# Kernel tuning notes

Hardware: AMD Instinct MI355X
Metric: run time of the kernel (lower is better)

Reference implementation:

```python
import jax, jax.numpy as jnp
import numpy as np
from jax import lax

# Mamba-2 block, mode='recurrent' (chunked SSD scan), default vanilla causal dwconv
D_MODEL = 2048
D_STATE = 64
D_CONV = 4
HEADDIM = 64
EXPAND = 2
NGROUPS = 1
CHUNK = 64
D_INNER = EXPAND * D_MODEL          # 4096
NHEADS = D_INNER // HEADDIM          # 64
CONV_DIM = D_INNER + 2 * NGROUPS * D_STATE   # 4224
D_IN_PROJ = 2 * D_INNER + 2 * NGROUPS * D_STATE + NHEADS  # 8384
BATCH, SEQ = 2, 4096
EPS = 1e-5


def setup_inputs() -> dict:
    key = jax.random.key(0)
    ks = jax.random.split(key, 8)
    x = jax.random.normal(ks[0], (BATCH, SEQ, D_MODEL), jnp.float32)
    in_proj_w = jax.random.normal(ks[1], (D_IN_PROJ, D_MODEL), jnp.float32) / np.sqrt(D_MODEL)
    conv_w = jax.random.normal(ks[2], (CONV_DIM, D_CONV), jnp.float32) / np.sqrt(D_CONV)
    conv_b = jnp.zeros((CONV_DIM,), jnp.float32)
    # dt_bias = inverse-softplus of dt sampled log-uniform in [1e-3, 1e-1]
    dt = jnp.exp(jax.random.uniform(ks[3], (NHEADS,)) * (np.log(0.1) - np.log(0.001)) + np.log(0.001))
    dt_bias = dt + jnp.log(-jnp.expm1(-dt))
    A_log = jnp.log(jax.random.uniform(ks[4], (NHEADS,), minval=1.0, maxval=16.0))
    D = jnp.ones((NHEADS,), jnp.float32)
    norm_w = jnp.ones((D_INNER,), jnp.float32)
    out_proj_w = jax.random.normal(ks[5], (D_MODEL, D_INNER), jnp.float32) / np.sqrt(D_INNER)
    return dict(x=x, in_proj_w=in_proj_w, conv_w=conv_w, conv_b=conv_b,
                dt_bias=dt_bias, A_log=A_log, D=D, norm_w=norm_w, out_proj_w=out_proj_w)


def _segsum(a):
    """a: (..., T) -> (..., T, T) lower-triangular segment sums."""
    T = a.shape[-1]
    cs = jnp.cumsum(a, axis=-1)
    d = cs[..., :, None] - cs[..., None, :]
    mask = jnp.tril(jnp.ones((T, T), dtype=bool))
    return jnp.where(mask, d, -jnp.inf)


def _forward(x, in_proj_w, conv_w, conv_b, dt_bias, A_log, D, norm_w, out_proj_w):
    Bsz, L, _ = x.shape
    nc = L // CHUNK
    zxbcdt = x @ in_proj_w.T                      # (B,L,D_IN_PROJ)
    z = zxbcdt[..., :D_INNER]
    xBC = zxbcdt[..., D_INNER:D_INNER + CONV_DIM]
    dt = zxbcdt[..., D_INNER + CONV_DIM:]         # (B,L,H)

    # causal depthwise conv1d (padding = d_conv-1, sliced to L) + SiLU
    xBC_t = jnp.transpose(xBC, (0, 2, 1))         # (B,C,L)
    y = lax.conv_general_dilated(xBC_t, conv_w[:, None, :], window_strides=(1,),
                                 padding=[(D_CONV - 1, 0)],
                                 feature_group_count=CONV_DIM,
                                 dimension_numbers=('NCH', 'OIH', 'NCH'))
    y = y + conv_b[None, :, None]
    xBC = jax.nn.silu(jnp.transpose(y, (0, 2, 1)))  # (B,L,C)

    xs = xBC[..., :D_INNER]
    Bm = xBC[..., D_INNER:D_INNER + NGROUPS * D_STATE]
    Cm = xBC[..., D_INNER + NGROUPS * D_STATE:]

    dt = jax.nn.softplus(dt + dt_bias)            # (B,L,H)
    A = -jnp.exp(A_log)                           # (H,)
    dA = dt * A                                   # (B,L,H)

    xh = xs.reshape(Bsz, L, NHEADS, HEADDIM)
    Bh = jnp.repeat(Bm.reshape(Bsz, L, NGROUPS, D_STATE), NHEADS // NGROUPS, axis=2)  # (B,L,H,N)
    Ch = jnp.repeat(Cm.reshape(Bsz, L, NGROUPS, D_STATE), NHEADS // NGROUPS, axis=2)
    xdt = xh * dt[..., None]                      # (B,L,H,P)

    # chunk
    Ac = dA.reshape(Bsz, nc, CHUNK, NHEADS).transpose(0, 1, 3, 2)  # (B,c,H,l)
    A_cumsum = jnp.cumsum(Ac, axis=-1)                             # (B,c,H,l)
    Lmat = jnp.exp(_segsum(Ac))                                    # (B,c,H,l,s)
    Cc = Ch.reshape(Bsz, nc, CHUNK, NHEADS, D_STATE)
    Bc = Bh.reshape(Bsz, nc, CHUNK, NHEADS, D_STATE)
    xc = xdt.reshape(Bsz, nc, CHUNK, NHEADS, HEADDIM)

    # intra-chunk (diagonal blocks)
    Y_diag = jnp.einsum('bclhn,bcshn,bchls,bcshp->bclhp', Cc, Bc, Lmat, xc)

    # per-chunk end states
    decay_states = jnp.exp(A_cumsum[..., -1:] - A_cumsum)          # (B,c,H,l)
    states = jnp.einsum('bcshn,bchs,bcshp->bchpn', Bc, decay_states, xc)  # (B,c,H,P,N)
    chunk_decay = jnp.exp(A_cumsum[..., -1])                       # (B,c,H)

    # inter-chunk recurrence over chunks
    def scan_fn(h, inp):
        dec, st = inp                              # (B,H), (B,H,P,N)
        prev = h
        h = dec[..., None, None] * h + st
        return h, prev

    h0 = jnp.zeros((Bsz, NHEADS, HEADDIM, D_STATE), x.dtype)
    _, prev_states = lax.scan(scan_fn, h0,
                              (chunk_decay.transpose(1, 0, 2), states.transpose(1, 0, 2, 3, 4)))
    prev_states = prev_states.transpose(1, 0, 2, 3, 4)             # (B,c,H,P,N)

    Y_off = jnp.einsum('bclhn,bchpn,bchl->bclhp', Cc, prev_states, jnp.exp(A_cumsum))

    Y = (Y_diag + Y_off).reshape(Bsz, L, NHEADS, HEADDIM) + D[:, None] * xh
    yf = Y.reshape(Bsz, L, D_INNER)

    # gated RMSNorm, then out projection
    yf = yf * jax.nn.silu(z)
    yf = yf * lax.rsqrt(jnp.mean(yf * yf, axis=-1, keepdims=True) + EPS) * norm_w
    return yf @ out_proj_w.T


def reference(x, in_proj_w, conv_w, conv_b, dt_bias, A_log, D, norm_w, out_proj_w):
    return _forward(x, in_proj_w, conv_w, conv_b, dt_bias, A_log, D, norm_w, out_proj_w)
```

## Files before the change

kernel.cpp:

```cpp
#include <hip/hip_runtime.h>

#define BATCH 2
#define SEQ 4096
#define DMODEL 2048
#define DINNER 4096
#define NHEADS 64
#define HEADDIM 64
#define DSTATE 64
#define CONVDIM 4224
#define DINPROJ 8384
#define NCHUNK 64
#define CHUNKL 64
#define MROWS (BATCH*SEQ)

typedef __bf16 bf16_t;
typedef bf16_t bf16x8 __attribute__((ext_vector_type(8)));
typedef float f32x4 __attribute__((ext_vector_type(4)));
typedef unsigned short u16;
typedef u16 u16x8 __attribute__((ext_vector_type(8)));

__device__ __forceinline__ u16 f2bf(float f) {
  unsigned int u = __float_as_uint(f);
  u += 0x7fff + ((u >> 16) & 1);
  return (u16)(u >> 16);
}
__device__ __forceinline__ float bf2f(u16 s) {
  return __uint_as_float(((unsigned int)s) << 16);
}

__device__ __forceinline__ void async_load16(const void* g, void* l) {
  __builtin_amdgcn_global_load_lds(
      (const __attribute__((address_space(1))) void*)g,
      (__attribute__((address_space(3))) void*)l, 16, 0, 0);
}

__global__ __launch_bounds__(256) void cvt_kernel(const float* __restrict__ in,
                                                  u16* __restrict__ out, int n4) {
  int i = blockIdx.x * 256 + threadIdx.x;
  if (i >= n4) return;
  float4 v = *(const float4*)(in + (size_t)i * 4);
  ushort4 o;
  o.x = f2bf(v.x); o.y = f2bf(v.y); o.z = f2bf(v.z); o.w = f2bf(v.w);
  *(ushort4*)(out + (size_t)i * 4) = o;
}

template <int EPI>
__global__ __launch_bounds__(512, 2) void gemm_bt(const u16* __restrict__ A,
                                                  const u16* __restrict__ B,
                                                  int M, int N, int K,
                                                  float* __restrict__ outf,
                                                  u16* __restrict__ z_out,
                                                  u16* __restrict__ xe_out,
                                                  float* __restrict__ bce_out,
                                                  float* __restrict__ dt_out) {
  __shared__ char smem[147456];
  const int tid = threadIdx.x;
  const int w = tid >> 6, lane = tid & 63;
  const int id = blockIdx.y * gridDim.x + blockIdx.x;
  const int xcd = id & 7;
  const int q = id >> 3;
  const int m0 = (xcd * 8 + (q & 7)) * 128;
  const int n0 = (q >> 3) * 256;
  const int wr = (w >> 2) * 64, wc = (w & 3) * 64;
  const int fr = lane & 15, fq = lane >> 4;
  const int nkt = K >> 6;

  const u16* aptr[2];
  const u16* bptr[4];
#pragma unroll
  for (int p = 0; p < 2; ++p) {
    int d = p * 8192 + tid * 16;
    int row = d >> 7;
    int colb = (d & 127) ^ ((row & 7) << 4);
    aptr[p] = A + (size_t)(m0 + row) * K + (colb >> 1);
  }
#pragma unroll
  for (int p = 0; p < 4; ++p) {
    int d = p * 8192 + tid * 16;
    int row = d >> 7;
    int colb = (d & 127) ^ ((row & 7) << 4);
    int gn = n0 + row;
    if (gn > N - 1) gn = N - 1;
    bptr[p] = B + (size_t)gn * K + (colb >> 1);
  }

  auto stage_to = [&](int bi) {
    char* base = (char*)smem + bi * 49152;
#pragma unroll
    for (int p = 0; p < 2; ++p) {
      async_load16(aptr[p], base + p * 8192 + tid * 16);
      aptr[p] += 64;
    }
#pragma unroll
    for (int p = 0; p < 4; ++p) {
      async_load16(bptr[p], base + 16384 + p * 8192 + tid * 16);
      bptr[p] += 64;
    }
  };

  auto load_frags = [&](int bi, int ks, bf16x8* af, bf16x8* bf) {
    const char* base = (const char*)smem + bi * 49152;
#pragma unroll
    for (int i = 0; i < 4; ++i) {
      int rowa = wr + i * 16 + fr;
      af[i] = *(const bf16x8*)(base + ((rowa * 128 + ks * 64 + fq * 16) ^ ((fr & 7) << 4)));
      int rowb = wc + i * 16 + fr;
      bf[i] = *(const bf16x8*)(base + 16384 +
                               ((rowb * 128 + ks * 64 + fq * 16) ^ ((fr & 7) << 4)));
    }
  };

  f32x4 acc[4][4];
#pragma unroll
  for (int i = 0; i < 4; ++i)
#pragma unroll
    for (int j = 0; j < 4; ++j) acc[i][j] = (f32x4){0.f, 0.f, 0.f, 0.f};

  stage_to(0);
  stage_to(1);
  asm volatile("s_waitcnt vmcnt(6)" ::: "memory");
  __builtin_amdgcn_s_barrier();

  bf16x8 a0[4], b0[4], a1[4], b1[4];
  load_frags(0, 0, a0, b0);

  int cur = 0;
  for (int t = 0; t < nkt; ++t) {
    int nx = cur + 1; if (nx == 3) nx = 0;
    int st = nx + 1; if (st == 3) st = 0;
    load_frags(cur, 1, a1, b1);
    const bool do_stage = (t + 2 < nkt);
    if (do_stage) stage_to(st);
    __builtin_amdgcn_s_setprio(1);
#pragma unroll
    for (int i = 0; i < 4; ++i)
#pragma unroll
      for (int j = 0; j < 4; ++j)
        acc[i][j] = __builtin_amdgcn_mfma_f32_16x16x32_bf16(a0[i], b0[j], acc[i][j], 0, 0, 0);
    __builtin_amdgcn_s_setprio(0);
    if (do_stage) {
      asm volatile("s_waitcnt vmcnt(6)" ::: "memory");
    } else {
      asm volatile("s_waitcnt vmcnt(0)" ::: "memory");
    }
    __builtin_amdgcn_s_barrier();
    if (t + 1 < nkt) load_frags(nx, 0, a0, b0);
    __builtin_amdgcn_s_setprio(1);
#pragma unroll
    for (int i = 0; i < 4; ++i)
#pragma unroll
      for (int j = 0; j < 4; ++j)
        acc[i][j] = __builtin_amdgcn_mfma_f32_16x16x32_bf16(a1[i], b1[j], acc[i][j], 0, 0, 0);
    __builtin_amdgcn_s_setprio(0);
    cur = nx;
  }

#pragma unroll
  for (int i = 0; i < 4; ++i) {
#pragma unroll
    for (int j = 0; j < 4; ++j) {
#pragma unroll
      for (int rr2 = 0; rr2 < 4; ++rr2) {
        int row = m0 + wr + i * 16 + fq * 4 + rr2;
        int col = n0 + wc + j * 16 + fr;
        float v = acc[i][j][rr2];
        if (EPI == 0) {
          if (col < N) outf[(size_t)row * N + col] = v;
        } else {
          if (col < DINNER) {
            z_out[(size_t)row * DINNER + col] = f2bf(v);
          } else if (col < 2 * DINNER) {
            xe_out[(size_t)row * DINNER + (col - DINNER)] = f2bf(v);
          } else if (col < DINNER + CONVDIM) {
            bce_out[(size_t)row * 128 + (col - 2 * DINNER)] = v;
          } else if (col < DINPROJ) {
            dt_out[(size_t)row * NHEADS + (col - DINNER - CONVDIM)] = v;
          }
        }
      }
    }
  }
}

__global__ __launch_bounds__(64) void dt_acs_kernel(float* __restrict__ dt,
                                                    const float* __restrict__ dt_bias,
                                                    const float* __restrict__ A_log,
                                                    float* __restrict__ Acs) {
  const int bid = blockIdx.x;
  const int h = threadIdx.x;
  const float bias = dt_bias[h];
  const float nA = -expf(A_log[h]);
  float run = 0.f;
  float* acs_row = Acs + ((size_t)bid * 64 + h) * 64;
  for (int s = 0; s < 64; ++s) {
    size_t g = ((size_t)bid * 64 + s) * 64 + h;
    float xv = dt[g] + bias;
    float sp = (xv > 20.f) ? xv : log1pf(expf(xv));
    dt[g] = sp;
    run += nA * sp;
    acs_row[s] = run;
  }
}

__global__ __launch_bounds__(256) void conv_silu_kernel(const u16* __restrict__ xe,
                                                        const float* __restrict__ bce,
                                                        const float* __restrict__ conv_w,
                                                        const float* __restrict__ conv_b,
                                                        u16* __restrict__ xs,
                                                        float* __restrict__ Bf,
                                                        float* __restrict__ Cf) {
  const int ch8 = blockIdx.x * 256 + threadIdx.x;
  if (ch8 >= CONVDIM / 8) return;
  const int b = blockIdx.z;
  const int l0 = blockIdx.y * 64;
  const int ch0 = ch8 * 8;
  const bool isx = ch0 < DINNER;
  float w[8][4], cb[8];
#pragma unroll
  for (int j = 0; j < 8; ++j) {
    cb[j] = conv_b[ch0 + j];
#pragma unroll
    for (int t = 0; t < 4; ++t) w[j][t] = conv_w[(ch0 + j) * 4 + t];
  }
  float win[3][8];
#pragma unroll
  for (int t = 0; t < 3; ++t) {
    int l = l0 - 3 + t;
    if (l < 0) {
#pragma unroll
      for (int j = 0; j < 8; ++j) win[t][j] = 0.f;
    } else if (isx) {
      const u16* p = &xe[((size_t)b * SEQ + l) * DINNER + ch0];
      ushort4 a = *(const ushort4*)p, bq = *(const ushort4*)(p + 4);
      win[t][0] = bf2f(a.x); win[t][1] = bf2f(a.y); win[t][2] = bf2f(a.z); win[t][3] = bf2f(a.w);
      win[t][4] = bf2f(bq.x); win[t][5] = bf2f(bq.y); win[t][6] = bf2f(bq.z); win[t][7] = bf2f(bq.w);
    } else {
      const float* p = &bce[((size_t)b * SEQ + l) * 128 + (ch0 - DINNER)];
      float4 a = *(const float4*)p, bq = *(const float4*)(p + 4);
      win[t][0] = a.x; win[t][1] = a.y; win[t][2] = a.z; win[t][3] = a.w;
      win[t][4] = bq.x; win[t][5] = bq.y; win[t][6] = bq.z; win[t][7] = bq.w;
    }
  }
  for (int li = 0; li < 64; ++li) {
    const int l = l0 + li;
    float cur[8];
    if (isx) {
      const u16* p = &xe[((size_t)b * SEQ + l) * DINNER + ch0];
      ushort4 a = *(const ushort4*)p, bq = *(const ushort4*)(p + 4);
      cur[0] = bf2f(a.x); cur[1] = bf2f(a.y); cur[2] = bf2f(a.z); cur[3] = bf2f(a.w);
      cur[4] = bf2f(bq.x); cur[5] = bf2f(bq.y); cur[6] = bf2f(bq.z); cur[7] = bf2f(bq.w);
    } else {
      const float* p = &bce[((size_t)b * SEQ + l) * 128 + (ch0 - DINNER)];
      float4 a = *(const float4*)p, bq = *(const float4*)(p + 4);
      cur[0] = a.x; cur[1] = a.y; cur[2] = a.z; cur[3] = a.w;
      cur[4] = bq.x; cur[5] = bq.y; cur[6] = bq.z; cur[7] = bq.w;
    }
    float o[8];
#pragma unroll
    for (int j = 0; j < 8; ++j) {
      float acc = cb[j] + w[j][0] * win[0][j] + w[j][1] * win[1][j] +
                  w[j][2] * win[2][j] + w[j][3] * cur[j];
      o[j] = acc / (1.f + expf(-acc));
    }
    if (isx) {
      const int h = ch0 >> 6, p0 = ch0 & 63;
      u16* dst = &xs[(((size_t)b * NHEADS + h) * SEQ + l) * 64 + p0];
      ushort4 s0, s1;
      s0.x = f2bf(o[0]); s0.y = f2bf(o[1]); s0.z = f2bf(o[2]); s0.w = f2bf(o[3]);
      s1.x = f2bf(o[4]); s1.y = f2bf(o[5]); s1.z = f2bf(o[6]); s1.w = f2bf(o[7]);
      *(ushort4*)dst = s0;
      *(ushort4*)(dst + 4) = s1;
    } else {
      const int c0 = ch0 - DINNER;
      float* dst = (c0 < DSTATE) ? &Bf[((size_t)b * SEQ + l) * 64 + c0]
                                 : &Cf[((size_t)b * SEQ + l) * 64 + (c0 - DSTATE)];
      float4 f0 = {o[0], o[1], o[2], o[3]}, f1 = {o[4], o[5], o[6], o[7]};
      *(float4*)dst = f0;
      *(float4*)(dst + 4) = f1;
    }
#pragma unroll
    for (int j = 0; j < 8; ++j) { win[0][j] = win[1][j]; win[1][j] = win[2][j]; win[2][j] = cur[j]; }
  }
}

__global__ __launch_bounds__(256) void states_kernel(const u16* __restrict__ xs,
                                                     const float* __restrict__ Bf,
                                                     const float* __restrict__ Acs,
                                                     const float* __restrict__ dtp,
                                                     u16* __restrict__ states) {
  const int bid = blockIdx.x;
  const int h = bid & 63, cc = (bid >> 6) & 63, b = bid >> 12;
  __shared__ float Xd[4096];
  __shared__ float Bl[4096];
  __shared__ float scale_s[64];
  const int tid = threadIdx.x;
  const float* acs = Acs + (size_t)bid * 64;
  if (tid < 64) {
    float alast = acs[63];
    scale_s[tid] = expf(alast - acs[tid]) * dtp[((size_t)b * SEQ + cc * 64 + tid) * 64 + h];
  }
  __syncthreads();
  {
    const int s = tid >> 2, q = (tid & 3) * 16;
    const float sc = scale_s[s];
    const u16* xp = &xs[(((size_t)b * NHEADS + h) * SEQ + cc * 64 + s) * 64 + q];
    const float* bp = &Bf[((size_t)b * SEQ + cc * 64 + s) * 64 + q];
#pragma unroll
    for (int k = 0; k < 4; ++k) {
      ushort4 xv = *(const ushort4*)(xp + k * 4);
      Xd[s * 64 + q + k * 4 + 0] = bf2f(xv.x) * sc;
      Xd[s * 64 + q + k * 4 + 1] = bf2f(xv.y) * sc;
      Xd[s * 64 + q + k * 4 + 2] = bf2f(xv.z) * sc;
      Xd[s * 64 + q + k * 4 + 3] = bf2f(xv.w) * sc;
      float4 bv = *(const float4*)(bp + k * 4);
      *(float4*)&Bl[s * 64 + q + k * 4] = bv;
    }
  }
  __syncthreads();
  const int p0 = (tid >> 4) * 4, n0 = (tid & 15) * 4;
  float av[4][4] = {};
  for (int s = 0; s < 64; ++s) {
    float4 xv = *(const float4*)&Xd[s * 64 + p0];
    float4 bv = *(const float4*)&Bl[s * 64 + n0];
    float xa[4] = {xv.x, xv.y, xv.z, xv.w};
    float ba[4] = {bv.x, bv.y, bv.z, bv.w};
#pragma unroll
    for (int i = 0; i < 4; ++i)
#pragma unroll
      for (int j = 0; j < 4; ++j) av[i][j] += xa[i] * ba[j];
  }
  u16* so = states + (size_t)bid * 4096;
#pragma unroll
  for (int i = 0; i < 4; ++i) {
    ushort4 o;
    o.x = f2bf(av[i][0]); o.y = f2bf(av[i][1]);
    o.z = f2bf(av[i][2]); o.w = f2bf(av[i][3]);
    *(ushort4*)&so[(p0 + i) * 64 + n0] = o;
  }
}

__global__ __launch_bounds__(256) void scan_kernel(u16* __restrict__ states,
                                                   const float* __restrict__ Acs) {
  int idx = blockIdx.x * 256 + threadIdx.x;
  int n = idx & 63, p = (idx >> 6) & 63, h = (idx >> 12) & 63, b = idx >> 18;
  float prev = 0.f;
  for (int c = 0; c < 64; ++c) {
    size_t bid = (size_t)(b * 64 + c) * 64 + h;
    size_t off = bid * 4096 + p * 64 + n;
    float sv = bf2f(states[off]);
    float cd = expf(Acs[bid * 64 + 63]);
    states[off] = f2bf(prev);
    prev = cd * prev + sv;
  }
}

__global__ __launch_bounds__(256) void cbt_kernel(const float* __restrict__ Bf,
                                                  const float* __restrict__ Cf,
                                                  float* __restrict__ cbt) {
  const int bc = blockIdx.x;
  __shared__ float Ct[64 * 65];
  __shared__ float Bt[64 * 65];
  const int tid = threadIdx.x;
  const size_t blbase = (size_t)(bc >> 6) * SEQ + (bc & 63) * 64;
  const int c4 = (tid & 15) * 4;
  for (int rr = tid >> 4; rr < 64; rr += 16) {
    float4 cv = *(const float4*)&Cf[(blbase + rr) * 64 + c4];
    float4 bv = *(const float4*)&Bf[(blbase + rr) * 64 + c4];
    Ct[rr * 65 + c4 + 0] = cv.x; Ct[rr * 65 + c4 + 1] = cv.y;
    Ct[rr * 65 + c4 + 2] = cv.z; Ct[rr * 65 + c4 + 3] = cv.w;
    Bt[rr * 65 + c4 + 0] = bv.x; Bt[rr * 65 + c4 + 1] = bv.y;
    Bt[rr * 65 + c4 + 2] = bv.z; Bt[rr * 65 + c4 + 3] = bv.w;
  }
  __syncthreads();
  const int l0 = (tid >> 4) * 4, s0 = (tid & 15) * 4;
  float a1[4][4] = {};
  for (int n = 0; n < 64; ++n) {
    float cv[4], bv[4];
#pragma unroll
    for (int i = 0; i < 4; ++i) { cv[i] = Ct[(l0 + i) * 65 + n]; bv[i] = Bt[(s0 + i) * 65 + n]; }
#pragma unroll
    for (int i = 0; i < 4; ++i)
#pragma unroll
      for (int j = 0; j < 4; ++j) a1[i][j] += cv[i] * bv[j];
  }
  float* dst = cbt + (size_t)bc * 4096;
#pragma unroll
  for (int i = 0; i < 4; ++i) {
    float4 o = {a1[i][0], a1[i][1], a1[i][2], a1[i][3]};
    *(float4*)&dst[(l0 + i) * 64 + s0] = o;
  }
}

__global__ __launch_bounds__(256) void y_kernel(const u16* __restrict__ xs,
                                                const float* __restrict__ cbt,
                                                const float* __restrict__ Cf,
                                                const float* __restrict__ Acs,
                                                const float* __restrict__ dtp,
                                                const u16* __restrict__ prev,
                                                const float* __restrict__ Dv,
                                                u16* __restrict__ zY) {
  const int bid = blockIdx.x;
  const int h = bid & 63, cc = (bid >> 6) & 63, b = bid >> 12;
  const int bc = bid >> 6;
  __shared__ char lds[32768 + 256];
  char* Cb = lds;
  char* Pb = lds + 8192;
  char* Sb = lds + 16384;
  char* Xb = lds + 24576;
  float* acsl = (float*)(lds + 32768);
  const int tid = threadIdx.x;
  const size_t blbase = (size_t)b * SEQ + cc * 64;
  if (tid < 64) acsl[tid] = Acs[(size_t)bid * 64 + tid];

  const int r = tid >> 2, c0 = (tid & 3) * 16;
  {
    const float* src = &Cf[(blbase + r) * 64 + c0];
    float4 a = *(const float4*)src, bq = *(const float4*)(src + 4);
    float4 c2 = *(const float4*)(src + 8), d2 = *(const float4*)(src + 12);
    u16x8 v0 = {f2bf(a.x), f2bf(a.y), f2bf(a.z), f2bf(a.w),
                f2bf(bq.x), f2bf(bq.y), f2bf(bq.z), f2bf(bq.w)};
    u16x8 v1 = {f2bf(c2.x), f2bf(c2.y), f2bf(c2.z), f2bf(c2.w),
                f2bf(d2.x), f2bf(d2.y), f2bf(d2.z), f2bf(d2.w)};
    *(u16x8*)(Cb + ((r * 128 + c0 * 2) ^ ((r & 7) << 4))) = v0;
    *(u16x8*)(Cb + ((r * 128 + c0 * 2 + 16) ^ ((r & 7) << 4))) = v1;
  }
  {
    const u16* src = &prev[(size_t)bid * 4096 + r * 64 + c0];
    u16x8 v0 = *(const u16x8*)src, v1 = *(const u16x8*)(src + 8);
    *(u16x8*)(Pb + ((r * 128 + c0 * 2) ^ ((r & 7) << 4))) = v0;
    *(u16x8*)(Pb + ((r * 128 + c0 * 2 + 16) ^ ((r & 7) << 4))) = v1;
  }
  {
    float dtv = dtp[(blbase + r) * 64 + h];
    const u16* src = &xs[(((size_t)b * NHEADS + h) * SEQ + cc * 64 + r) * 64 + c0];
    u16x8 x0 = *(const u16x8*)src, x1 = *(const u16x8*)(src + 8);
#pragma unroll
    for (int k = 0; k < 16; ++k) {
      u16 xv = (k < 8) ? x0[k] : x1[k - 8];
      u16 o = f2bf(bf2f(xv) * dtv);
      int p = c0 + k;
      *(u16*)(Xb + ((p * 128 + r * 2) ^ ((p & 7) << 4))) = o;
    }
  }
  __syncthreads();
  {
    float al = acsl[r];
    const float* src = &cbt[(size_t)bc * 4096 + r * 64 + c0];
    u16 ov[16];
#pragma unroll
    for (int k = 0; k < 16; ++k) {
      int s = c0 + k;
      float v = (r >= s) ? src[k] * expf(al - acsl[s]) : 0.f;
      ov[k] = f2bf(v);
    }
    u16x8 v0 = {ov[0], ov[1], ov[2], ov[3], ov[4], ov[5], ov[6], ov[7]};
    u16x8 v1 = {ov[8], ov[9], ov[10], ov[11], ov[12], ov[13], ov[14], ov[15]};
    *(u16x8*)(Sb + ((r * 128 + c0 * 2) ^ ((r & 7) << 4))) = v0;
    *(u16x8*)(Sb + ((r * 128 + c0 * 2 + 16) ^ ((r & 7) << 4))) = v1;
  }
  __syncthreads();

  const int w = tid >> 6, lane = tid & 63;
  const int fr = lane & 15, fq = lane >> 4;
  const int lw = w * 16;
  auto ldf = [&](const char* base, int row, int ks) -> bf16x8 {
    return *(const bf16x8*)(base + ((row * 128 + ks * 64 + fq * 16) ^ ((row & 7) << 4)));
  };
  bf16x8 aS[2], aC[2];
#pragma unroll
  for (int ks = 0; ks < 2; ++ks) {
    aS[ks] = ldf(Sb, lw + fr, ks);
    aC[ks] = ldf(Cb, lw + fr, ks);
  }
  f32x4 ay[4], ao[4];
#pragma unroll
  for (int j = 0; j < 4; ++j) { ay[j] = (f32x4){0.f,0.f,0.f,0.f}; ao[j] = (f32x4){0.f,0.f,0.f,0.f}; }
#pragma unroll
  for (int j = 0; j < 4; ++j) {
#pragma unroll
    for (int ks = 0; ks < 2; ++ks) {
      bf16x8 bX = ldf(Xb, j * 16 + fr, ks);
      ay[j] = __builtin_amdgcn_mfma_f32_16x16x32_bf16(aS[ks], bX, ay[j], 0, 0, 0);
      bf16x8 bP = ldf(Pb, j * 16 + fr, ks);
      ao[j] = __builtin_amdgcn_mfma_f32_16x16x32_bf16(aC[ks], bP, ao[j], 0, 0, 0);
    }
  }
  const float Dh = Dv[h];
  float el[4];
#pragma unroll
  for (int reg = 0; reg < 4; ++reg) el[reg] = expf(acsl[lw + fq * 4 + reg]);
#pragma unroll
  for (int j = 0; j < 4; ++j) {
#pragma unroll
    for (int reg = 0; reg < 4; ++reg) {
      int l = lw + fq * 4 + reg, p = j * 16 + fr;
      float yv = ay[j][reg] + el[reg] * ao[j][reg] +
                 Dh * bf2f(xs[(((size_t)b * NHEADS + h) * SEQ + cc * 64 + l) * 64 + p]);
      size_t zoff = (blbase + l) * DINNER + h * 64 + p;
      float zv = bf2f(zY[zoff]);
      zY[zoff] = f2bf(yv * (zv / (1.f + expf(-zv))));
    }
  }
}

__global__ __launch_bounds__(256) void rms_kernel(const u16* __restrict__ Y,
                                                  const float* __restrict__ nw,
                                                  u16* __restrict__ yf) {
  const int row = blockIdx.x, tid = threadIdx.x;
  const u16* yrow = Y + (size_t)row * DINNER;
  float g[16];
  float ss = 0.f;
#pragma unroll
  for (int i = 0; i < 4; ++i) {
    ushort4 yv = *(const ushort4*)&yrow[tid * 16 + i * 4];
    float ya[4] = {bf2f(yv.x), bf2f(yv.y), bf2f(yv.z), bf2f(yv.w)};
#pragma unroll
    for (int j = 0; j < 4; ++j) {
      g[i * 4 + j] = ya[j];
      ss += ya[j] * ya[j];
    }
  }
#pragma unroll
  for (int off = 32; off > 0; off >>= 1) ss += __shfl_down(ss, off, 64);
  __shared__ float red[4];
  if ((tid & 63) == 0) red[tid >> 6] = ss;
  __syncthreads();
  float tot = red[0] + red[1] + red[2] + red[3];
  float sc = rsqrtf(tot * (1.f / (float)DINNER) + 1e-5f);
#pragma unroll
  for (int i = 0; i < 4; ++i) {
    float4 nv = *(const float4*)&nw[tid * 16 + i * 4];
    float na[4] = {nv.x, nv.y, nv.z, nv.w};
    ushort4 o;
    o.x = f2bf(g[i * 4 + 0] * sc * na[0]);
    o.y = f2bf(g[i * 4 + 1] * sc * na[1]);
    o.z = f2bf(g[i * 4 + 2] * sc * na[2]);
    o.w = f2bf(g[i * 4 + 3] * sc * na[3]);
    *(ushort4*)&yf[(size_t)row * DINNER + tid * 16 + i * 4] = o;
  }
}

extern "C" void kernel_launch(void* const* d_in, const int* in_sizes, int n_in,
                              void* d_out, int out_size, void* d_ws, size_t ws_size,
                              hipStream_t stream) {
  const float* x = (const float*)d_in[0];
  const float* in_proj_w = (const float*)d_in[1];
  const float* conv_w = (const float*)d_in[2];
  const float* conv_b = (const float*)d_in[3];
  const float* dt_bias = (const float*)d_in[4];
  const float* A_log = (const float*)d_in[5];
  const float* Dvec = (const float*)d_in[6];
  const float* norm_w = (const float*)d_in[7];
  const float* out_proj_w = (const float*)d_in[8];

  char* ws = (char*)d_ws;
  u16* xbf    = (u16*)(ws + 0);
  u16* winbf  = (u16*)(ws + 33554432);
  u16* xs     = (u16*)(ws + 0);
  u16* yfbf   = (u16*)(ws + 0);
  u16* zY     = (u16*)(ws + 67895296);
  u16* xe     = (u16*)(ws + 135004160);
  u16* statesb= (u16*)(ws + 135004160);
  u16* woutbf = (u16*)(ws + 135004160);
  float* bce  = (float*)(ws + 202113024);
  float* dtb  = (float*)(ws + 206307328);
  float* Acs  = (float*)(ws + 208404480);
  float* Bfb  = (float*)(ws + 210501632);
  float* Cfb  = (float*)(ws + 212598784);
  float* cbt  = (float*)(ws + 214695936);

  cvt_kernel<<<16384, 256, 0, stream>>>(x, xbf, 4194304);
  cvt_kernel<<<16768, 256, 0, stream>>>(in_proj_w, winbf, 4292608);

  gemm_bt<1><<<dim3(64, 33), 512, 0, stream>>>(xbf, winbf, MROWS, DINPROJ, DMODEL,
                                               nullptr, zY, xe, bce, dtb);

  dt_acs_kernel<<<128, 64, 0, stream>>>(dtb, dt_bias, A_log, Acs);

  conv_silu_kernel<<<dim3(3, 64, 2), 256, 0, stream>>>(xe, bce, conv_w, conv_b, xs, Bfb, Cfb);

  states_kernel<<<8192, 256, 0, stream>>>(xs, Bfb, Acs, dtb, statesb);
  scan_kernel<<<2048, 256, 0, stream>>>(statesb, Acs);
  cbt_kernel<<<128, 256, 0, stream>>>(Bfb, Cfb, cbt);
  y_kernel<<<8192, 256, 0, stream>>>(xs, cbt, Cfb, Acs, dtb, statesb, Dvec, zY);

  rms_kernel<<<8192, 256, 0, stream>>>(zY, norm_w, yfbf);

  cvt_kernel<<<8192, 256, 0, stream>>>(out_proj_w, woutbf, 2097152);
  gemm_bt<0><<<dim3(64, 8), 512, 0, stream>>>(yfbf, woutbf, MROWS, DMODEL, DINNER,
                                              (float*)d_out, nullptr, nullptr, nullptr, nullptr);
}
```

Baseline: 801.1 us.

## Use MFMA for chunk states, halve conv rows per block, remap out-proj tiles

The states kernel now stages scaled X and B as bf16 in swizzled shared memory and computes the 64x64 chunk state with bf16 MFMA instructions, replacing the scalar FP32 outer-product loop. The conv kernel processes 32 sequence rows per block instead of 64 and launches twice as many blocks for more parallelism. The output-projection GEMM switches to a simpler N-fastest tile mapping instead of the XCD-aware swizzle. The MFMA path rounds the decay-scaled inputs to bf16, which loses some precision.

```diff
diff --git a/kernel.cpp b/kernel.cpp
--- a/kernel.cpp
+++ b/kernel.cpp
@@ -57,10 +57,16 @@
   const int tid = threadIdx.x;
   const int w = tid >> 6, lane = tid & 63;
   const int id = blockIdx.y * gridDim.x + blockIdx.x;
-  const int xcd = id & 7;
-  const int q = id >> 3;
-  const int m0 = (xcd * 8 + (q & 7)) * 128;
-  const int n0 = (q >> 3) * 256;
+  int m0, n0;
+  if (EPI == 0) {
+    n0 = (id & 7) * 256;
+    m0 = (id >> 3) * 128;
+  } else {
+    const int xcd = id & 7;
+    const int q = id >> 3;
+    m0 = (xcd * 8 + (q & 7)) * 128;
+    n0 = (q >> 3) * 256;
+  }
   const int wr = (w >> 2) * 64, wc = (w & 3) * 64;
   const int fr = lane & 15, fq = lane >> 4;
   const int nkt = K >> 6;
@@ -212,7 +218,7 @@
   const int ch8 = blockIdx.x * 256 + threadIdx.x;
   if (ch8 >= CONVDIM / 8) return;
   const int b = blockIdx.z;
-  const int l0 = blockIdx.y * 64;
+  const int l0 = blockIdx.y * 32;
   const int ch0 = ch8 * 8;
   const bool isx = ch0 < DINNER;
   float w[8][4], cb[8];
@@ -241,7 +247,7 @@
       win[t][4] = bq.x; win[t][5] = bq.y; win[t][6] = bq.z; win[t][7] = bq.w;
     }
   }
-  for (int li = 0; li < 64; ++li) {
+  for (int li = 0; li < 32; ++li) {
     const int l = l0 + li;
     float cur[8];
     if (isx) {
@@ -290,53 +296,60 @@
                                                      u16* __restrict__ states) {
   const int bid = blockIdx.x;
   const int h = bid & 63, cc = (bid >> 6) & 63, b = bid >> 12;
-  __shared__ float Xd[4096];
-  __shared__ float Bl[4096];
-  __shared__ float scale_s[64];
+  __shared__ char lds[16384 + 256];
+  char* Axb = lds;
+  char* Bb = lds + 8192;
+  float* scale_s = (float*)(lds + 16384);
   const int tid = threadIdx.x;
   const float* acs = Acs + (size_t)bid * 64;
+  const size_t blbase = (size_t)b * SEQ + cc * 64;
   if (tid < 64) {
     float alast = acs[63];
-    scale_s[tid] = expf(alast - acs[tid]) * dtp[((size_t)b * SEQ + cc * 64 + tid) * 64 + h];
+    scale_s[tid] = expf(alast - acs[tid]) * dtp[(blbase + tid) * 64 + h];
   }
   __syncthreads();
+  const int r = tid >> 2, c0 = (tid & 3) * 16;
   {
-    const int s = tid >> 2, q = (tid & 3) * 16;
-    const float sc = scale_s[s];
-    const u16* xp = &xs[(((size_t)b * NHEADS + h) * SEQ + cc * 64 + s) * 64 + q];
-    const float* bp = &Bf[((size_t)b * SEQ + cc * 64 + s) * 64 + q];
-#pragma unroll
-    for (int k = 0; k < 4; ++k) {
-      ushort4 xv = *(const ushort4*)(xp + k * 4);
-      Xd[s * 64 + q + k * 4 + 0] = bf2f(xv.x) * sc;
-      Xd[s * 64 + q + k * 4 + 1] = bf2f(xv.y) * sc;
-      Xd[s * 64 + q + k * 4 + 2] = bf2f(xv.z) * sc;
-      Xd[s * 64 + q + k * 4 + 3] = bf2f(xv.w) * sc;
-      float4 bv = *(const float4*)(bp + k * 4);
-      *(float4*)&Bl[s * 64 + q + k * 4] = bv;
+    const float sc = scale_s[r];
+    const u16* src = &xs[(((size_t)b * NHEADS + h) * SEQ + cc * 64 + r) * 64 + c0];
+    u16x8 x0 = *(const u16x8*)src, x1 = *(const u16x8*)(src + 8);
+    const float* bsrc = &Bf[(blbase + r) * 64 + c0];
+    float4 bv0 = *(const float4*)bsrc, bv1 = *(const float4*)(bsrc + 4);
+    float4 bv2 = *(const float4*)(bsrc + 8), bv3 = *(const float4*)(bsrc + 12);
+    float ba[16] = {bv0.x, bv0.y, bv0.z, bv0.w, bv1.x, bv1.y, bv1.z, bv1.w,
+                    bv2.x, bv2.y, bv2.z, bv2.w, bv3.x, bv3.y, bv3.z, bv3.w};
+#pragma unroll
+    for (int k = 0; k < 16; ++k) {
+      u16 xv = (k < 8) ? x0[k] : x1[k - 8];
+      int p = c0 + k;
+      *(u16*)(Axb + ((p * 128 + r * 2) ^ ((p & 7) << 4))) = f2bf(bf2f(xv) * sc);
+      *(u16*)(Bb + ((p * 128 + r * 2) ^ ((p & 7) << 4))) = f2bf(ba[k]);
     }
   }
   __syncthreads();
-  const int p0 = (tid >> 4) * 4, n0 = (tid & 15) * 4;
-  float av[4][4] = {};
-  for (int s = 0; s < 64; ++s) {
-    float4 xv = *(const float4*)&Xd[s * 64 + p0];
-    float4 bv = *(const float4*)&Bl[s * 64 + n0];
-    float xa[4] = {xv.x, xv.y, xv.z, xv.w};
-    float ba[4] = {bv.x, bv.y, bv.z, bv.w};
-#pragma unroll
-    for (int i = 0; i < 4; ++i)
-#pragma unroll
-      for (int j = 0; j < 4; ++j) av[i][j] += xa[i] * ba[j];
-  }
+  const int w = tid >> 6, lane = tid & 63;
+  const int fr = lane & 15, fq = lane >> 4;
+  const int pw = w * 16;
+  auto ldf = [&](const char* base, int row, int ks) -> bf16x8 {
+    return *(const bf16x8*)(base + ((row * 128 + ks * 64 + fq * 16) ^ ((row & 7) << 4)));
+  };
+  bf16x8 aA[2];
+  aA[0] = ldf(Axb, pw + fr, 0);
+  aA[1] = ldf(Axb, pw + fr, 1);
+  f32x4 acc[4];
+#pragma unroll
+  for (int j = 0; j < 4; ++j) acc[j] = (f32x4){0.f, 0.f, 0.f, 0.f};
+#pragma unroll
+  for (int j = 0; j < 4; ++j)
+#pragma unroll
+    for (int ks = 0; ks < 2; ++ks)
+      acc[j] = __builtin_amdgcn_mfma_f32_16x16x32_bf16(aA[ks], ldf(Bb, j * 16 + fr, ks), acc[j], 0, 0, 0);
   u16* so = states + (size_t)bid * 4096;
 #pragma unroll
-  for (int i = 0; i < 4; ++i) {
-    ushort4 o;
-    o.x = f2bf(av[i][0]); o.y = f2bf(av[i][1]);
-    o.z = f2bf(av[i][2]); o.w = f2bf(av[i][3]);
-    *(ushort4*)&so[(p0 + i) * 64 + n0] = o;
-  }
+  for (int j = 0; j < 4; ++j)
+#pragma unroll
+    for (int reg = 0; reg < 4; ++reg)
+      so[(pw + fq * 4 + reg) * 64 + j * 16 + fr] = f2bf(acc[j][reg]);
 }
 
 __global__ __launch_bounds__(256) void scan_kernel(u16* __restrict__ states,
@@ -577,7 +590,7 @@
 
   dt_acs_kernel<<<128, 64, 0, stream>>>(dtb, dt_bias, A_log, Acs);
 
-  conv_silu_kernel<<<dim3(3, 64, 2), 256, 0, stream>>>(xe, bce, conv_w, conv_b, xs, Bfb, Cfb);
+  conv_silu_kernel<<<dim3(3, 128, 2), 256, 0, stream>>>(xe, bce, conv_w, conv_b, xs, Bfb, Cfb);
 
   states_kernel<<<8192, 256, 0, stream>>>(xs, Bfb, Acs, dtb, statesb);
   scan_kernel<<<2048, 256, 0, stream>>>(statesb, Acs);
```

After: 744.1 us. 1.08x faster.
